# Kernel tuning notes

Measured on AMD Instinct MI355X. Metric: run time of the kernel, lower is better.

## Reference

```python
import jax, jax.numpy as jnp
import numpy as np

B = 1024      # batch of samples accumulated
F_DIM = 768   # backbone feature dim (ViT out_dim)
M = 512       # buffer_size (random projection width)
C = 100       # number of classes


def setup_inputs() -> dict:
    key = jax.random.key(0)
    k1, k2, k3 = jax.random.split(key, 3)
    X = jax.random.normal(k1, (B, F_DIM), dtype=jnp.float32)
    # RandomBuffer weight (fixed random projection), Linear-style init scale
    W = jax.random.normal(k2, (F_DIM, M), dtype=jnp.float32) / np.float32(np.sqrt(F_DIM))
    labels = jax.random.randint(k3, (B,), 0, C)  # argmax(Y, dim=1)
    return {"X": X, "W": W, "labels": labels}


def reference(X, W, labels):
    # RandomBuffer.forward: relu(X @ W) -> [B, M]
    feat = jax.nn.relu(X @ W)
    # per-sample outer product f^T f, scatter-added per class label
    outer = feat[:, :, None] * feat[:, None, :]          # [B, M, M]
    phi = jax.ops.segment_sum(outer, labels, num_segments=C)   # [C, M, M]
    mu = jax.ops.segment_sum(feat, labels, num_segments=C)     # [C, M]
    count = jax.ops.segment_sum(jnp.ones((B,), feat.dtype), labels, num_segments=C)  # [C]
    return phi, mu, count
```

## Files before the change

### kernel.cpp

```cpp
#include <hip/hip_runtime.h>

#define B_N    1024
#define F_DIMC 768
#define M_DIM  512
#define C_N    100
#define KSTEP  32
#define NSTEP  (F_DIMC / KSTEP)
#define NGEMM  512
#define NIDX   25

typedef float f32x4 __attribute__((ext_vector_type(4)));
typedef short s16x8 __attribute__((ext_vector_type(8)));

__device__ __forceinline__ unsigned int f2bf(float x) {
  unsigned int u = __builtin_bit_cast(unsigned int, x);
  return (u + 0x7fffu + ((u >> 16) & 1u)) >> 16;
}
__device__ __forceinline__ float bf2f(unsigned int h) {
  return __builtin_bit_cast(float, h << 16);
}

__global__ __launch_bounds__(256) void gemm_index_kernel(
    const float* __restrict__ X, const float* __restrict__ W,
    const int* __restrict__ labels, float* __restrict__ feat,
    int* __restrict__ counts, int* __restrict__ idx) {
  __shared__ unsigned short Ah[2][32][40], Al[2][32][40];
  __shared__ unsigned short Bh[2][32][40], Bl[2][32][40];
  __shared__ int lab[B_N];

  const int t = threadIdx.x;
  const int b = (int)blockIdx.x;

  if (b >= NGEMM) {
    for (int i = t; i < B_N; i += 256) lab[i] = labels[i];
    __syncthreads();
    const int w    = t >> 6;
    const int lane = t & 63;
    const int c    = (b - NGEMM) * 4 + w;
    if (c < C_N) {
      int base = 0;
      for (int ch = 0; ch < 16; ++ch) {
        const int j = ch * 64 + lane;
        const bool hit = (lab[j] == c);
        const unsigned long long mask = __ballot(hit);
        if (hit) {
          const int r = __popcll(mask & ((1ull << lane) - 1ull));
          idx[c * B_N + base + r] = j;
        }
        base += __popcll(mask);
      }
      if (lane == 0) counts[c] = base;
    }
    return;
  }

  const int bm = (b >> 4) * 32;
  const int bn = (b & 15) * 32;

  const bool isX = (t < 128);
  const int xr = t >> 2;
  const int xk = (t & 3) * 8;
  const int uu = isX ? 0 : (t - 128);
  const int wk = (uu >> 3) * 2;
  const int wc = (uu & 7) * 4;

  const float* __restrict__ Xp = X + (size_t)(bm + xr) * F_DIMC + xk;
  const float* __restrict__ Wp = W + (size_t)wk * M_DIM + bn + wc;

  const int lane = t & 63;
  const int wv   = t >> 6;
  const int m0 = (wv & 1) * 16;
  const int n0 = (wv >> 1) * 16;
  const int fr = lane & 15;
  const int fq = (lane >> 4) * 8;

  f32x4 acc = {0.f, 0.f, 0.f, 0.f};

  float4 ra0, ra1, rb0, rb1;
  if (isX) {
    ra0 = *(const float4*)(Xp);
    ra1 = *(const float4*)(Xp + 4);
  } else {
    rb0 = *(const float4*)(Wp);
    rb1 = *(const float4*)(Wp + M_DIM);
  }

  auto STAGE = [&](int buf) {
    if (isX) {
      const float v[8] = {ra0.x, ra0.y, ra0.z, ra0.w,
                          ra1.x, ra1.y, ra1.z, ra1.w};
      s16x8 hv, lv;
#pragma unroll
      for (int j = 0; j < 8; ++j) {
        const unsigned int hb = f2bf(v[j]);
        hv[j] = (short)hb;
        lv[j] = (short)f2bf(v[j] - bf2f(hb));
      }
      *(s16x8*)&Ah[buf][xr][xk] = hv;
      *(s16x8*)&Al[buf][xr][xk] = lv;
    } else {
      const float a[4] = {rb0.x, rb0.y, rb0.z, rb0.w};
      const float d[4] = {rb1.x, rb1.y, rb1.z, rb1.w};
#pragma unroll
      for (int i = 0; i < 4; ++i) {
        const unsigned int ha = f2bf(a[i]), hd = f2bf(d[i]);
        const unsigned int la = f2bf(a[i] - bf2f(ha));
        const unsigned int ld = f2bf(d[i] - bf2f(hd));
        *(unsigned int*)&Bh[buf][wc + i][wk] = ha | (hd << 16);
        *(unsigned int*)&Bl[buf][wc + i][wk] = la | (ld << 16);
      }
    }
  };

  STAGE(0);
  __syncthreads();

  for (int it = 0; it < NSTEP; ++it) {
    const int cur = it & 1;
    if (it + 1 < NSTEP) {
      const int k0 = (it + 1) * KSTEP;
      if (isX) {
        ra0 = *(const float4*)(Xp + k0);
        ra1 = *(const float4*)(Xp + k0 + 4);
      } else {
        rb0 = *(const float4*)(Wp + (size_t)k0 * M_DIM);
        rb1 = *(const float4*)(Wp + (size_t)(k0 + 1) * M_DIM);
      }
    }
    const s16x8 ah = *(const s16x8*)&Ah[cur][m0 + fr][fq];
    const s16x8 al = *(const s16x8*)&Al[cur][m0 + fr][fq];
    const s16x8 bh = *(const s16x8*)&Bh[cur][n0 + fr][fq];
    const s16x8 bl = *(const s16x8*)&Bl[cur][n0 + fr][fq];
    acc = __builtin_amdgcn_mfma_f32_16x16x32_bf16(ah, bh, acc, 0, 0, 0);
    acc = __builtin_amdgcn_mfma_f32_16x16x32_bf16(al, bh, acc, 0, 0, 0);
    acc = __builtin_amdgcn_mfma_f32_16x16x32_bf16(ah, bl, acc, 0, 0, 0);
    if (it + 1 < NSTEP) STAGE(cur ^ 1);
    __syncthreads();
  }

  const int r0 = (lane >> 4) * 4;
#pragma unroll
  for (int r = 0; r < 4; ++r)
    feat[(size_t)(bm + m0 + r0 + r) * M_DIM + bn + n0 + fr] =
        fmaxf(acc[r], 0.0f);
}

__global__ __launch_bounds__(256, 4) void phi_mu_kernel(
    const float* __restrict__ feat, const int* __restrict__ counts,
    const int* __restrict__ idx, float* __restrict__ phi,
    float* __restrict__ mu, float* __restrict__ cnt_out) {
  const int c = blockIdx.y;
  const int n = counts[c];
  const int* __restrict__ id = idx + c * B_N;
  const int t = threadIdx.x;

  if (blockIdx.x == 16) {
    float2 acc = make_float2(0.f, 0.f);
    for (int s = 0; s < n; ++s) {
      const float2 q = *(const float2*)&feat[(size_t)id[s] * M_DIM + t * 2];
      acc.x += q.x;
      acc.y += q.y;
    }
    *(float2*)&mu[(size_t)c * M_DIM + t * 2] = acc;
    if (t == 0) cnt_out[c] = (float)n;
    return;
  }

  const int px = (int)blockIdx.x;
  const int tr = t >> 6;
  const int tc = t & 63;

  __shared__ float F[16][M_DIM];

  float acc[8][8] = {};

  for (int s0 = 0; s0 < n; s0 += 16) {
    const int chunk  = min(16, n - s0);
    if (s0) __syncthreads();
    const int nslots = chunk << 7;
    for (int v = t; v < nslots; v += 256) {
      const int sl = v >> 7;
      const int fp = (v & 127) << 2;
      *(float4*)&F[sl][fp] =
          *(const float4*)&feat[(size_t)id[s0 + sl] * M_DIM + fp];
    }
    __syncthreads();
    for (int sl = 0; sl < chunk; ++sl) {
      const float4 a0 = *(const float4*)&F[sl][px * 32 + tr * 8];
      const float4 a1 = *(const float4*)&F[sl][px * 32 + tr * 8 + 4];
      const float4 b0 = *(const float4*)&F[sl][tc * 4];
      const float4 b1 = *(const float4*)&F[sl][256 + tc * 4];
      const float av[8] = {a0.x, a0.y, a0.z, a0.w, a1.x, a1.y, a1.z, a1.w};
      const float bv[8] = {b0.x, b0.y, b0.z, b0.w, b1.x, b1.y, b1.z, b1.w};
#pragma unroll
      for (int r = 0; r < 8; ++r)
#pragma unroll
        for (int q = 0; q < 8; ++q)
          acc[r][q] += av[r] * bv[q];
    }
  }

  float* __restrict__ out = phi + (size_t)c * M_DIM * M_DIM;
#pragma unroll
  for (int r = 0; r < 8; ++r) {
    const size_t row = (size_t)(px * 32 + tr * 8 + r) * M_DIM;
    const f32x4 o0 = {acc[r][0], acc[r][1], acc[r][2], acc[r][3]};
    const f32x4 o1 = {acc[r][4], acc[r][5], acc[r][6], acc[r][7]};
    __builtin_nontemporal_store(o0, (f32x4*)&out[row + tc * 4]);
    __builtin_nontemporal_store(o1, (f32x4*)&out[row + 256 + tc * 4]);
  }
}

extern "C" void kernel_launch(void* const* d_in, const int* in_sizes, int n_in,
                              void* d_out, int out_size, void* d_ws,
                              size_t ws_size, hipStream_t stream) {
  const float* X      = (const float*)d_in[0];
  const float* W      = (const float*)d_in[1];
  const int*   labels = (const int*)d_in[2];

  float* out = (float*)d_out;
  float* phi = out;
  float* mu  = out + (size_t)C_N * M_DIM * M_DIM;
  float* cnt = mu + (size_t)C_N * M_DIM;

  float* feat   = (float*)d_ws;
  int*   counts = (int*)((char*)d_ws + (size_t)B_N * M_DIM * sizeof(float));
  int*   idx    = counts + 128;

  hipLaunchKernelGGL(gemm_index_kernel, dim3(NGEMM + NIDX), dim3(256), 0,
                     stream, X, W, labels, feat, counts, idx);
  hipLaunchKernelGGL(phi_mu_kernel, dim3(17, C_N), dim3(256), 0, stream,
                     feat, counts, idx, phi, mu, cnt);
}
```

Before: 42.69 us.

## Make phi kernel persistent with register prefetch of next unit's feature rows

The phi/mu kernel now runs as a persistent grid of 850 blocks, each looping over two (class, sub-tile) work units. While a block finishes one unit and writes its output, it prefetches the first 16 gathered feature rows for its next unit into registers, so the gather latency overlaps the large nontemporal phi stores. This adds register pressure (8 float4 per thread), halves the number of blocks in flight, and removes the occupancy hint from launch bounds.

```diff
diff --git a/kernel.cpp b/kernel.cpp
--- a/kernel.cpp
+++ b/kernel.cpp
@@ -8,6 +8,8 @@
 #define NSTEP  (F_DIMC / KSTEP)
 #define NGEMM  512
 #define NIDX   25
+#define NUNITS (17 * C_N)
+#define PBLK   850
 
 typedef float f32x4 __attribute__((ext_vector_type(4)));
 typedef short s16x8 __attribute__((ext_vector_type(8)));
@@ -145,69 +147,123 @@
         fmaxf(acc[r], 0.0f);
 }
 
-__global__ __launch_bounds__(256, 4) void phi_mu_kernel(
+__global__ __launch_bounds__(256) void phi_mu_kernel(
     const float* __restrict__ feat, const int* __restrict__ counts,
     const int* __restrict__ idx, float* __restrict__ phi,
     float* __restrict__ mu, float* __restrict__ cnt_out) {
-  const int c = blockIdx.y;
-  const int n = counts[c];
-  const int* __restrict__ id = idx + c * B_N;
+  __shared__ float F[16][M_DIM];
   const int t = threadIdx.x;
-
-  if (blockIdx.x == 16) {
-    float2 acc = make_float2(0.f, 0.f);
-    for (int s = 0; s < n; ++s) {
-      const float2 q = *(const float2*)&feat[(size_t)id[s] * M_DIM + t * 2];
-      acc.x += q.x;
-      acc.y += q.y;
-    }
-    *(float2*)&mu[(size_t)c * M_DIM + t * 2] = acc;
-    if (t == 0) cnt_out[c] = (float)n;
-    return;
-  }
-
-  const int px = (int)blockIdx.x;
-  const int tr = t >> 6;
-  const int tc = t & 63;
-
-  __shared__ float F[16][M_DIM];
-
-  float acc[8][8] = {};
-
-  for (int s0 = 0; s0 < n; s0 += 16) {
-    const int chunk  = min(16, n - s0);
-    if (s0) __syncthreads();
-    const int nslots = chunk << 7;
-    for (int v = t; v < nslots; v += 256) {
+  const int b = (int)blockIdx.x;
+
+  float4 pf[8];
+
+  auto PREFETCH = [&](int u) {
+    if (u >= NUNITS) return;
+    const int c = u / 17, sub = u % 17;
+    if (sub == 16) return;
+    const int n = counts[c];
+    const int chunk = n < 16 ? n : 16;
+    const int* __restrict__ id = idx + c * B_N;
+#pragma unroll
+    for (int i = 0; i < 8; ++i) {
+      const int v  = t + (i << 8);
       const int sl = v >> 7;
-      const int fp = (v & 127) << 2;
-      *(float4*)&F[sl][fp] =
-          *(const float4*)&feat[(size_t)id[s0 + sl] * M_DIM + fp];
+      if (sl < chunk) {
+        const int fp = (v & 127) << 2;
+        pf[i] = *(const float4*)&feat[(size_t)id[sl] * M_DIM + fp];
+      }
+    }
+  };
+
+  PREFETCH(b);
+
+  for (int u = b; u < NUNITS; u += PBLK) {
+    const int c   = u / 17;
+    const int sub = u - c * 17;
+    const int n = counts[c];
+    const int* __restrict__ id = idx + c * B_N;
+
+    if (sub == 16) {
+      float2 acc = make_float2(0.f, 0.f);
+      for (int s = 0; s < n; ++s) {
+        const float2 q = *(const float2*)&feat[(size_t)id[s] * M_DIM + t * 2];
+        acc.x += q.x;
+        acc.y += q.y;
+      }
+      PREFETCH(u + PBLK);
+      *(float2*)&mu[(size_t)c * M_DIM + t * 2] = acc;
+      if (t == 0) cnt_out[c] = (float)n;
+      continue;
+    }
+
+    const int px = sub;
+    const int tr = t >> 6;
+    const int tc = t & 63;
+
+    float acc[8][8] = {};
+
+    {
+      const int chunk = n < 16 ? n : 16;
+#pragma unroll
+      for (int i = 0; i < 8; ++i) {
+        const int v  = t + (i << 8);
+        const int sl = v >> 7;
+        if (sl < chunk) *(float4*)&F[sl][(v & 127) << 2] = pf[i];
+      }
+      __syncthreads();
+      for (int sl = 0; sl < chunk; ++sl) {
+        const float4 a0 = *(const float4*)&F[sl][px * 32 + tr * 8];
+        const float4 a1 = *(const float4*)&F[sl][px * 32 + tr * 8 + 4];
+        const float4 b0 = *(const float4*)&F[sl][tc * 4];
+        const float4 b1 = *(const float4*)&F[sl][256 + tc * 4];
+        const float av[8] = {a0.x, a0.y, a0.z, a0.w, a1.x, a1.y, a1.z, a1.w};
+        const float bv[8] = {b0.x, b0.y, b0.z, b0.w, b1.x, b1.y, b1.z, b1.w};
+#pragma unroll
+        for (int r = 0; r < 8; ++r)
+#pragma unroll
+          for (int q = 0; q < 8; ++q)
+            acc[r][q] += av[r] * bv[q];
+      }
+    }
+
+    for (int s0 = 16; s0 < n; s0 += 16) {
+      const int chunk = min(16, n - s0);
+      __syncthreads();
+      const int nslots = chunk << 7;
+      for (int v = t; v < nslots; v += 256) {
+        const int sl = v >> 7;
+        const int fp = (v & 127) << 2;
+        *(float4*)&F[sl][fp] =
+            *(const float4*)&feat[(size_t)id[s0 + sl] * M_DIM + fp];
+      }
+      __syncthreads();
+      for (int sl = 0; sl < chunk; ++sl) {
+        const float4 a0 = *(const float4*)&F[sl][px * 32 + tr * 8];
+        const float4 a1 = *(const float4*)&F[sl][px * 32 + tr * 8 + 4];
+        const float4 b0 = *(const float4*)&F[sl][tc * 4];
+        const float4 b1 = *(const float4*)&F[sl][256 + tc * 4];
+        const float av[8] = {a0.x, a0.y, a0.z, a0.w, a1.x, a1.y, a1.z, a1.w};
+        const float bv[8] = {b0.x, b0.y, b0.z, b0.w, b1.x, b1.y, b1.z, b1.w};
+#pragma unroll
+        for (int r = 0; r < 8; ++r)
+#pragma unroll
+          for (int q = 0; q < 8; ++q)
+            acc[r][q] += av[r] * bv[q];
+      }
+    }
+
+    PREFETCH(u + PBLK);
+
+    float* __restrict__ out = phi + (size_t)c * M_DIM * M_DIM;
+#pragma unroll
+    for (int r = 0; r < 8; ++r) {
+      const size_t row = (size_t)(px * 32 + tr * 8 + r) * M_DIM;
+      const f32x4 o0 = {acc[r][0], acc[r][1], acc[r][2], acc[r][3]};
+      const f32x4 o1 = {acc[r][4], acc[r][5], acc[r][6], acc[r][7]};
+      __builtin_nontemporal_store(o0, (f32x4*)&out[row + tc * 4]);
+      __builtin_nontemporal_store(o1, (f32x4*)&out[row + 256 + tc * 4]);
     }
     __syncthreads();
-    for (int sl = 0; sl < chunk; ++sl) {
-      const float4 a0 = *(const float4*)&F[sl][px * 32 + tr * 8];
-      const float4 a1 = *(const float4*)&F[sl][px * 32 + tr * 8 + 4];
-      const float4 b0 = *(const float4*)&F[sl][tc * 4];
-      const float4 b1 = *(const float4*)&F[sl][256 + tc * 4];
-      const float av[8] = {a0.x, a0.y, a0.z, a0.w, a1.x, a1.y, a1.z, a1.w};
-      const float bv[8] = {b0.x, b0.y, b0.z, b0.w, b1.x, b1.y, b1.z, b1.w};
-#pragma unroll
-      for (int r = 0; r < 8; ++r)
-#pragma unroll
-        for (int q = 0; q < 8; ++q)
-          acc[r][q] += av[r] * bv[q];
-    }
-  }
-
-  float* __restrict__ out = phi + (size_t)c * M_DIM * M_DIM;
-#pragma unroll
-  for (int r = 0; r < 8; ++r) {
-    const size_t row = (size_t)(px * 32 + tr * 8 + r) * M_DIM;
-    const f32x4 o0 = {acc[r][0], acc[r][1], acc[r][2], acc[r][3]};
-    const f32x4 o1 = {acc[r][4], acc[r][5], acc[r][6], acc[r][7]};
-    __builtin_nontemporal_store(o0, (f32x4*)&out[row + tc * 4]);
-    __builtin_nontemporal_store(o1, (f32x4*)&out[row + 256 + tc * 4]);
   }
 }
 
@@ -229,6 +285,6 @@
 
   hipLaunchKernelGGL(gemm_index_kernel, dim3(NGEMM + NIDX), dim3(256), 0,
                      stream, X, W, labels, feat, counts, idx);
-  hipLaunchKernelGGL(phi_mu_kernel, dim3(17, C_N), dim3(256), 0, stream,
+  hipLaunchKernelGGL(phi_mu_kernel, dim3(PBLK), dim3(256), 0, stream,
                      feat, counts, idx, phi, mu, cnt);
 }
```

Measured after the change: 50.31 us. 1.18x slower.
